# Kernel optimization log

Measured on AMD Instinct MI355X. Metric: run time of the kernel, lower is better.

The kernel has to match this reference:

```python
import jax, jax.numpy as jnp
import numpy as np

DIM = 1024
NUM_HEADS = 16
SCALE = (DIM // NUM_HEADS) ** -0.5


def setup_inputs() -> dict:
    key = jax.random.key(0)
    k1, k2, k3, k4 = jax.random.split(key, 4)
    x = jax.random.normal(k1, (8, 2048, DIM), dtype=jnp.float32)
    # nn.Linear(dim, 3*dim, bias=False): weight [3*dim, dim]
    w_qkv = jax.random.normal(k2, (3 * DIM, DIM), dtype=jnp.float32) * (DIM ** -0.5)
    # nn.Linear(dim, dim): weight [dim, dim], bias [dim]
    w_out = jax.random.normal(k3, (DIM, DIM), dtype=jnp.float32) * (DIM ** -0.5)
    b_out = jax.random.normal(k4, (DIM,), dtype=jnp.float32) * 0.01
    return {"x": x, "w_qkv": w_qkv, "w_out": w_out, "b_out": b_out}


def reference(x, w_qkv, w_out, b_out):
    # qkv projection: x @ w_qkv.T -> [B, N, 3*dim]; chunk into q,k,v
    qkv = jnp.einsum('bnd,ed->bne', x, w_qkv)
    q, k, v = jnp.split(qkv, 3, axis=-1)
    # full attention over the whole dim (module never splits heads)
    attn = jnp.einsum('bnd,bmd->bnm', q, k) * SCALE  # [B, N, N]
    attn = jax.nn.softmax(attn, axis=-1)
    out = jnp.einsum('bnm,bmd->bnd', attn, v)
    return jnp.einsum('bnd,ed->bne', out, w_out) + b_out
```

## Files before the change

### kernel.cpp

```cpp
#include <hip/hip_runtime.h>
#include <hip/hip_bf16.h>
#include <cstdint>
#include <cstddef>


typedef __bf16 bf16x8 __attribute__((ext_vector_type(8)));
typedef float f32x4 __attribute__((ext_vector_type(4)));

__device__ __forceinline__ void gl_lds16(const void* g, void* l) {
  __builtin_amdgcn_global_load_lds((const __attribute__((address_space(1))) void*)g,
                                   (__attribute__((address_space(3))) void*)l, 16, 0, 0);
}

__global__ __launch_bounds__(256) void cast_f32_bf16(const float* __restrict__ in,
                                                     __hip_bfloat16* __restrict__ out, int n) {
  int i = (blockIdx.x * 256 + threadIdx.x) * 8;
  if (i >= n) return;
  float4 a = *(const float4*)(in + i);
  float4 b = *(const float4*)(in + i + 4);
  __align__(16) __hip_bfloat16 o[8];
  o[0] = __float2bfloat16(a.x); o[1] = __float2bfloat16(a.y);
  o[2] = __float2bfloat16(a.z); o[3] = __float2bfloat16(a.w);
  o[4] = __float2bfloat16(b.x); o[5] = __float2bfloat16(b.y);
  o[6] = __float2bfloat16(b.z); o[7] = __float2bfloat16(b.w);
  *(uint4*)(out + i) = *(const uint4*)o;
}

#define STAGE_(SRCP, OFFS, LDSBASE, TT, KS)                                        \
  if ((TT) < NT) {                                                                 \
    const int kb_ = (TT) * 64 + (KS) * 32;                                         \
    _Pragma("unroll") for (int i = 0; i < 2; ++i)                                  \
      gl_lds16((SRCP) + OFFS[i] + kb_,                                             \
               sm + (LDSBASE) + (size_t)(tid + 512 * i) * 8);                      \
  }

#define PHASE_(APL, BPL, CH, LOADB, DOVM, ...)                                     \
  {                                                                                \
    const __hip_bfloat16* Ap_ = sm + (APL) * 8192;                                 \
    _Pragma("unroll") for (int mi = 0; mi < 4; ++mi)                               \
      af[mi] = *(const bf16x8*)(Ap_ + arow + ((CH) * 4 + mi) * 512);               \
    if (LOADB) {                                                                   \
      const __hip_bfloat16* Bp_ = sm + 32768 + (BPL) * 8192;                       \
      _Pragma("unroll") for (int ni = 0; ni < 4; ++ni)                             \
        bfr[ni] = *(const bf16x8*)(Bp_ + brow + ni * 512);                         \
    }                                                                              \
    __VA_ARGS__;                                                                   \
    __builtin_amdgcn_s_barrier();                                                  \
    asm volatile("s_waitcnt lgkmcnt(0)" ::: "memory");                             \
    __builtin_amdgcn_sched_barrier(0);                                             \
    __builtin_amdgcn_s_setprio(1);                                                 \
    _Pragma("unroll") for (int mi = 0; mi < 4; ++mi)                               \
      _Pragma("unroll") for (int ni = 0; ni < 4; ++ni)                             \
        acc[(CH) * 4 + mi][ni] = __builtin_amdgcn_mfma_f32_16x16x32_bf16(          \
            af[mi], bfr[ni], acc[(CH) * 4 + mi][ni], 0, 0, 0);                     \
    __builtin_amdgcn_s_setprio(0);                                                 \
    if (DOVM) asm volatile("s_waitcnt vmcnt(8)" ::: "memory");                     \
    __builtin_amdgcn_s_barrier();                                                  \
  }

#define GEMM_CORE256(APTR, LDA, BPTR, LDB, KLEN)                                   \
  __shared__ __align__(16) __hip_bfloat16 sm[65536];                  \
  const __hip_bfloat16* Abase_ = (APTR);                                           \
  const __hip_bfloat16* Bbase_ = (BPTR);                                           \
  const int tid  = threadIdx.x;                                                    \
  const int lane = tid & 63;                                                       \
  const int q    = lane >> 4;                                                      \
  const int m16  = lane & 15;                                                      \
  const int wave = tid >> 6;                                                       \
  const int wr   = wave >> 2;                                                      \
  const int wc   = wave & 3;                                                       \
  const int row0 = blockIdx.y * 256;                                               \
  const int col0 = blockIdx.x * 256;                                               \
    \
    \
  unsigned srcA[2], srcB[2];                                                       \
  _Pragma("unroll") for (int i = 0; i < 2; ++i) {                                  \
    const int c_ = tid + 512 * i;                                                  \
    const int r_ = c_ >> 2;                                                        \
    const int kc_ = ((c_ & 3) ^ ((r_ >> 1) & 3)) * 8;                              \
    srcA[i] = (unsigned)(row0 + r_) * (unsigned)(LDA) + (unsigned)kc_;             \
    srcB[i] = (unsigned)(col0 + r_) * (unsigned)(LDB) + (unsigned)kc_;             \
  }                                                                                \
  const int NT = (KLEN) >> 6;                                                      \
  f32x4 acc[8][4];                                                                 \
  { const f32x4 z_ = {0.f, 0.f, 0.f, 0.f};                                         \
    _Pragma("unroll") for (int i = 0; i < 8; ++i)                                  \
      _Pragma("unroll") for (int j = 0; j < 4; ++j) acc[i][j] = z_; }              \
            \
  const int soff = (q ^ ((m16 >> 1) & 3)) * 8;                                     \
  const int arow = (wr * 128 + m16) * 32 + soff;                                   \
  const int brow = (wc * 64 + m16) * 32 + soff;                                    \
  bf16x8 af[4], bfr[4];                                                            \
     \
  STAGE_(Abase_, srcA, 0,             0, 0)                                        \
  STAGE_(Bbase_, srcB, 32768 + 0,     0, 0)                                        \
  STAGE_(Abase_, srcA, 8192,          0, 1)                                        \
  STAGE_(Bbase_, srcB, 32768 + 8192,  0, 1)                                        \
  STAGE_(Abase_, srcA, 16384,         1, 0)                                        \
  STAGE_(Bbase_, srcB, 32768 + 16384, 1, 0)                                        \
  asm volatile("s_waitcnt vmcnt(8)" ::: "memory");                                 \
  __builtin_amdgcn_s_barrier();                                                    \
  for (int t = 0; t < NT; t += 2) {                                                \
                                            \
    PHASE_(0, 0, 0, 1, 0, STAGE_(Abase_, srcA, 24576,         t + 1, 1))           \
    PHASE_(0, 0, 1, 0, 1, STAGE_(Bbase_, srcB, 32768 + 24576, t + 1, 1))           \
    PHASE_(1, 1, 0, 1, 0, STAGE_(Abase_, srcA, 0,             t + 2, 0))           \
    PHASE_(1, 1, 1, 0, 1, STAGE_(Bbase_, srcB, 32768 + 0,     t + 2, 0))           \
                                          \
    PHASE_(2, 2, 0, 1, 0, STAGE_(Abase_, srcA, 8192,          t + 2, 1))           \
    PHASE_(2, 2, 1, 0, 1, STAGE_(Bbase_, srcB, 32768 + 8192,  t + 2, 1))           \
    PHASE_(3, 3, 0, 1, 0, STAGE_(Abase_, srcA, 16384,         t + 3, 0))           \
    PHASE_(3, 3, 1, 0, 1, STAGE_(Bbase_, srcB, 32768 + 16384, t + 3, 0))           \
  }                                                                                \
                 \
  const int crow = row0 + wr * 128 + q * 4;                                        \
  const int ccol = col0 + wc * 64 + m16;

template<int OUT_MODE>
__global__ __launch_bounds__(512) void gemm_bt(
    const __hip_bfloat16* __restrict__ A, int lda, long long sA,
    const __hip_bfloat16* __restrict__ B, int ldb, long long sB,
    void* __restrict__ Cv, int ldc, long long sC,
    const float* __restrict__ bias, const float* __restrict__ rsum, int K)
{
  const int bz = blockIdx.z;
  GEMM_CORE256(A + (size_t)bz * sA, lda, B + (size_t)bz * sB, ldb, K)
  if constexpr (OUT_MODE == 0) {
    __hip_bfloat16* C = (__hip_bfloat16*)Cv + (size_t)bz * sC;
    #pragma unroll
    for (int mi = 0; mi < 8; ++mi)
      #pragma unroll
      for (int ni = 0; ni < 4; ++ni)
        #pragma unroll
        for (int r = 0; r < 4; ++r)
          C[(size_t)(crow + mi * 16 + r) * ldc + ccol + ni * 16] = __float2bfloat16(acc[mi][ni][r]);
  } else {
    float* C = (float*)Cv + (size_t)bz * sC;
    float bv[4];
    #pragma unroll
    for (int ni = 0; ni < 4; ++ni) bv[ni] = bias[ccol + ni * 16];
    #pragma unroll
    for (int mi = 0; mi < 8; ++mi) {
      float sc[4];
      #pragma unroll
      for (int r = 0; r < 4; ++r) sc[r] = 1.f / rsum[crow + mi * 16 + r];
      #pragma unroll
      for (int ni = 0; ni < 4; ++ni)
        #pragma unroll
        for (int r = 0; r < 4; ++r)
          C[(size_t)(crow + mi * 16 + r) * ldc + ccol + ni * 16] =
              acc[mi][ni][r] * sc[r] + bv[ni];
    }
  }
}

__global__ __launch_bounds__(512) void gemm_qk_exp(
    const __hip_bfloat16* __restrict__ A, int lda, long long sA,
    const __hip_bfloat16* __restrict__ B, int ldb, long long sB,
    __hip_bfloat16* __restrict__ Pv, int ldc, long long sC,
    float* __restrict__ Lsum, int ldl, int K)
{
  const int bz = blockIdx.z;
  GEMM_CORE256(A + (size_t)bz * sA, lda, B + (size_t)bz * sB, ldb, K)
  __hip_bfloat16* C = Pv + (size_t)bz * sC;
  float* Lrow = Lsum + (size_t)bz * ldl;
  #pragma unroll
  for (int mi = 0; mi < 8; ++mi) {
    #pragma unroll
    for (int r = 0; r < 4; ++r) {
      float s = 0.f;
      #pragma unroll
      for (int ni = 0; ni < 4; ++ni) {
        const float e = __expf(acc[mi][ni][r] * 0.125f);
        const __hip_bfloat16 h = __float2bfloat16(e);
        C[(size_t)(crow + mi * 16 + r) * ldc + ccol + ni * 16] = h;
        s += __bfloat162float(h);
      }
      #pragma unroll
      for (int mask = 1; mask < 16; mask <<= 1) s += __shfl_xor(s, mask);
      if (m16 == 0) atomicAdd(&Lrow[crow + mi * 16 + r], s);
    }
  }
}

__global__ __launch_bounds__(512) void gemm_qkv(
    const __hip_bfloat16* __restrict__ A, int lda,
    const __hip_bfloat16* __restrict__ B, int ldb,
    __hip_bfloat16* __restrict__ QK,
    __hip_bfloat16* __restrict__ Vt, int M, int K)
{
  GEMM_CORE256(A, lda, B, ldb, K)
  if (blockIdx.x < 8) {
    #pragma unroll
    for (int mi = 0; mi < 8; ++mi)
      #pragma unroll
      for (int ni = 0; ni < 4; ++ni)
        #pragma unroll
        for (int r = 0; r < 4; ++r)
          QK[(size_t)(crow + mi * 16 + r) * 2048 + ccol + ni * 16] = __float2bfloat16(acc[mi][ni][r]);
  } else {
    #pragma unroll
    for (int mi = 0; mi < 8; ++mi) {
      const int rowbase = crow + mi * 16;
      #pragma unroll
      for (int ni = 0; ni < 4; ++ni) {
        const int vc = ccol + ni * 16 - 2048;
        __align__(8) __hip_bfloat16 o[4];
        #pragma unroll
        for (int r = 0; r < 4; ++r) o[r] = __float2bfloat16(acc[mi][ni][r]);
        *(uint2*)(Vt + (size_t)vc * M + rowbase) = *(const uint2*)o;
      }
    }
  }
}

extern "C" void kernel_launch(void* const* d_in, const int* in_sizes, int n_in,
                              void* d_out, int out_size, void* d_ws, size_t ws_size,
                              hipStream_t stream) {
  const float* x     = (const float*)d_in[0];
  const float* w_qkv = (const float*)d_in[1];
  const float* w_out = (const float*)d_in[2];
  const float* b_out = (const float*)d_in[3];
  float* out = (float*)d_out;

  constexpr int Bz = 8, N = 2048, D = 1024, E = 3 * D;
  constexpr int M = Bz * N;

  char* p = (char*)d_ws;
  __hip_bfloat16* Wo = (__hip_bfloat16*)p; p += (size_t)D * D * 2;
  __hip_bfloat16* Vt = (__hip_bfloat16*)p; p += (size_t)D * M * 2;
  __hip_bfloat16* QK = (__hip_bfloat16*)p; p += (size_t)M * 2 * D * 2;
  __hip_bfloat16* AO = (__hip_bfloat16*)p; p += (size_t)M * D * 2;
  float*          L  = (float*)p;          p += (size_t)M * 4;
  char* dyn = p;
  const size_t fixed_sz = (size_t)(dyn - (char*)d_ws);
  const size_t xw_sz = (size_t)M * D * 2 + (size_t)E * D * 2;

  int G = 1;
  for (int g = 8; g >= 1; g >>= 1) {
    size_t dyn_sz = (size_t)g * N * N * 2;
    if (dyn_sz < xw_sz) dyn_sz = xw_sz;
    if (fixed_sz + dyn_sz <= ws_size) { G = g; break; }
  }

  __hip_bfloat16* Xb = (__hip_bfloat16*)dyn;
  __hip_bfloat16* Wq = (__hip_bfloat16*)(dyn + (size_t)M * D * 2);
  __hip_bfloat16* P  = (__hip_bfloat16*)dyn;

  hipMemsetAsync(L, 0, (size_t)M * 4, stream);
  cast_f32_bf16<<<(M * D) / (8 * 256), 256, 0, stream>>>(x, Xb, M * D);
  cast_f32_bf16<<<(E * D) / (8 * 256), 256, 0, stream>>>(w_qkv, Wq, E * D);
  cast_f32_bf16<<<(D * D) / (8 * 256), 256, 0, stream>>>(w_out, Wo, D * D);
  gemm_qkv<<<dim3(E / 256, M / 256), 512, 0, stream>>>(Xb, D, Wq, D, QK, Vt, M, D);

  for (int g = 0; g < Bz / G; ++g) {
    const __hip_bfloat16* Qg = QK + (size_t)g * G * N * (2 * D);
    gemm_qk_exp<<<dim3(N / 256, N / 256, G), 512, 0, stream>>>(
        Qg, 2 * D, (long long)N * 2 * D,
        Qg + D, 2 * D, (long long)N * 2 * D,
        P, N, (long long)N * N,
        L + (size_t)g * G * N, N, D);
    gemm_bt<0><<<dim3(D / 256, N / 256, G), 512, 0, stream>>>(
        P, N, (long long)N * N,
        Vt + (size_t)g * G * N, M, (long long)N,
        AO + (size_t)g * G * N * D, D, (long long)N * D,
        nullptr, nullptr, N);
  }

  gemm_bt<2><<<dim3(D / 256, M / 256, 1), 512, 0, stream>>>(
      AO, D, 0LL, Wo, D, 0LL, out, D, 0LL, b_out, L, D);
}
```

Baseline: 426.4 us.

## Double-buffer LDS fragments in registers and drop per-phase barrier in GEMM loop

```diff
diff --git a/kernel.cpp b/kernel.cpp
--- a/kernel.cpp
+++ b/kernel.cpp
@@ -26,6 +26,7 @@
   *(uint4*)(out + i) = *(const uint4*)o;
 }
 
+
 #define STAGE_(SRCP, OFFS, LDSBASE, TT, KS)                                        \
   if ((TT) < NT) {                                                                 \
     const int kb_ = (TT) * 64 + (KS) * 32;                                         \
@@ -34,29 +35,24 @@
                sm + (LDSBASE) + (size_t)(tid + 512 * i) * 8);                      \
   }
 
-#define PHASE_(APL, BPL, CH, LOADB, DOVM, ...)                                     \
-  {                                                                                \
-    const __hip_bfloat16* Ap_ = sm + (APL) * 8192;                                 \
-    _Pragma("unroll") for (int mi = 0; mi < 4; ++mi)                               \
-      af[mi] = *(const bf16x8*)(Ap_ + arow + ((CH) * 4 + mi) * 512);               \
-    if (LOADB) {                                                                   \
-      const __hip_bfloat16* Bp_ = sm + 32768 + (BPL) * 8192;                       \
-      _Pragma("unroll") for (int ni = 0; ni < 4; ++ni)                             \
-        bfr[ni] = *(const bf16x8*)(Bp_ + brow + ni * 512);                         \
-    }                                                                              \
-    __VA_ARGS__;                                                                   \
-    __builtin_amdgcn_s_barrier();                                                  \
-    asm volatile("s_waitcnt lgkmcnt(0)" ::: "memory");                             \
-    __builtin_amdgcn_sched_barrier(0);                                             \
-    __builtin_amdgcn_s_setprio(1);                                                 \
-    _Pragma("unroll") for (int mi = 0; mi < 4; ++mi)                               \
-      _Pragma("unroll") for (int ni = 0; ni < 4; ++ni)                             \
-        acc[(CH) * 4 + mi][ni] = __builtin_amdgcn_mfma_f32_16x16x32_bf16(          \
-            af[mi], bfr[ni], acc[(CH) * 4 + mi][ni], 0, 0, 0);                     \
-    __builtin_amdgcn_s_setprio(0);                                                 \
-    if (DOVM) asm volatile("s_waitcnt vmcnt(8)" ::: "memory");                     \
-    __builtin_amdgcn_s_barrier();                                                  \
-  }
+#define LDA_FRAGS(BUF, APL, CH)                                                    \
+  _Pragma("unroll") for (int mi = 0; mi < 4; ++mi)                                 \
+    af[BUF][mi] = *(const bf16x8*)(sm + (APL) * 8192 + arow + ((CH) * 4 + mi) * 512);
+#define LDB_FRAGS(BUF, BPL)                                                        \
+  _Pragma("unroll") for (int ni = 0; ni < 4; ++ni)                                 \
+    bfr[BUF][ni] = *(const bf16x8*)(sm + 32768 + (BPL) * 8192 + brow + ni * 512);
+
+#define MFMA16(AB, BB, CH)                                                         \
+  __builtin_amdgcn_s_setprio(1);                                                   \
+  _Pragma("unroll") for (int mi = 0; mi < 4; ++mi)                                 \
+    _Pragma("unroll") for (int ni = 0; ni < 4; ++ni)                               \
+      acc[(CH) * 4 + mi][ni] = __builtin_amdgcn_mfma_f32_16x16x32_bf16(            \
+          af[AB][mi], bfr[BB][ni], acc[(CH) * 4 + mi][ni], 0, 0, 0);               \
+  __builtin_amdgcn_s_setprio(0);
+
+#define PHEND()                                                                    \
+  asm volatile("s_waitcnt vmcnt(6)" ::: "memory");                                 \
+  __builtin_amdgcn_s_barrier();
 
 #define GEMM_CORE256(APTR, LDA, BPTR, LDB, KLEN)                                   \
   __shared__ __align__(16) __hip_bfloat16 sm[65536];                  \
@@ -71,8 +67,6 @@
   const int wc   = wave & 3;                                                       \
   const int row0 = blockIdx.y * 256;                                               \
   const int col0 = blockIdx.x * 256;                                               \
-    \
-    \
   unsigned srcA[2], srcB[2];                                                       \
   _Pragma("unroll") for (int i = 0; i < 2; ++i) {                                  \
     const int c_ = tid + 512 * i;                                                  \
@@ -86,31 +80,45 @@
   { const f32x4 z_ = {0.f, 0.f, 0.f, 0.f};                                         \
     _Pragma("unroll") for (int i = 0; i < 8; ++i)                                  \
       _Pragma("unroll") for (int j = 0; j < 4; ++j) acc[i][j] = z_; }              \
-            \
   const int soff = (q ^ ((m16 >> 1) & 3)) * 8;                                     \
   const int arow = (wr * 128 + m16) * 32 + soff;                                   \
   const int brow = (wc * 64 + m16) * 32 + soff;                                    \
-  bf16x8 af[4], bfr[4];                                                            \
-     \
+  bf16x8 af[2][4], bfr[2][4];                                                      \
+       \
   STAGE_(Abase_, srcA, 0,             0, 0)                                        \
-  STAGE_(Bbase_, srcB, 32768 + 0,     0, 0)                                        \
+  STAGE_(Bbase_, srcB, 32768,         0, 0)                                        \
   STAGE_(Abase_, srcA, 8192,          0, 1)                                        \
   STAGE_(Bbase_, srcB, 32768 + 8192,  0, 1)                                        \
   STAGE_(Abase_, srcA, 16384,         1, 0)                                        \
   STAGE_(Bbase_, srcB, 32768 + 16384, 1, 0)                                        \
-  asm volatile("s_waitcnt vmcnt(8)" ::: "memory");                                 \
+  asm volatile("s_waitcnt vmcnt(8)" ::: "memory");           \
   __builtin_amdgcn_s_barrier();                                                    \
+  LDA_FRAGS(0, 0, 0) LDB_FRAGS(0, 0)                             \
   for (int t = 0; t < NT; t += 2) {                                                \
-                                            \
-    PHASE_(0, 0, 0, 1, 0, STAGE_(Abase_, srcA, 24576,         t + 1, 1))           \
-    PHASE_(0, 0, 1, 0, 1, STAGE_(Bbase_, srcB, 32768 + 24576, t + 1, 1))           \
-    PHASE_(1, 1, 0, 1, 0, STAGE_(Abase_, srcA, 0,             t + 2, 0))           \
-    PHASE_(1, 1, 1, 0, 1, STAGE_(Bbase_, srcB, 32768 + 0,     t + 2, 0))           \
-                                          \
-    PHASE_(2, 2, 0, 1, 0, STAGE_(Abase_, srcA, 8192,          t + 2, 1))           \
-    PHASE_(2, 2, 1, 0, 1, STAGE_(Bbase_, srcB, 32768 + 8192,  t + 2, 1))           \
-    PHASE_(3, 3, 0, 1, 0, STAGE_(Abase_, srcA, 16384,         t + 3, 0))           \
-    PHASE_(3, 3, 1, 0, 1, STAGE_(Bbase_, srcB, 32768 + 16384, t + 3, 0))           \
+                  \
+    LDA_FRAGS(1, 0, 1)                 STAGE_(Abase_, srcA, 24576,         t+1, 1) \
+    MFMA16(0, 0, 0) PHEND()                                                        \
+                       \
+    LDA_FRAGS(0, 1, 0) LDB_FRAGS(1, 1) STAGE_(Bbase_, srcB, 32768 + 24576, t+1, 1) \
+    MFMA16(1, 0, 1) PHEND()                                                        \
+                  \
+    LDA_FRAGS(1, 1, 1)                 STAGE_(Abase_, srcA, 0,             t+2, 0) \
+    MFMA16(0, 1, 0) PHEND()                                                        \
+                       \
+    LDA_FRAGS(0, 2, 0) LDB_FRAGS(0, 2) STAGE_(Bbase_, srcB, 32768,         t+2, 0) \
+    MFMA16(1, 1, 1) PHEND()                                                        \
+                  \
+    LDA_FRAGS(1, 2, 1)                 STAGE_(Abase_, srcA, 8192,          t+2, 1) \
+    MFMA16(0, 0, 0) PHEND()                                                        \
+                       \
+    LDA_FRAGS(0, 3, 0) LDB_FRAGS(1, 3) STAGE_(Bbase_, srcB, 32768 + 8192,  t+2, 1) \
+    MFMA16(1, 0, 1) PHEND()                                                        \
+                  \
+    LDA_FRAGS(1, 3, 1)                 STAGE_(Abase_, srcA, 16384,         t+3, 0) \
+    MFMA16(0, 1, 0) PHEND()                                                        \
+             \
+    LDA_FRAGS(0, 0, 0) LDB_FRAGS(0, 0) STAGE_(Bbase_, srcB, 32768 + 16384, t+3, 0) \
+    MFMA16(1, 1, 1) PHEND()                                                        \
   }                                                                                \
                  \
   const int crow = row0 + wr * 128 + q * 4;                                        \
```

After: 590.9 us. 38.6% more time.
